# Kernel optimization log

Measured on AMD Instinct MI355X. Metric: run time of the kernel, lower is better.

The kernel has to match this reference:

```python
import jax, jax.numpy as jnp
import numpy as np

K_SIZE = 5
PAD = 2  # (dilation*(k-1)+1 - stride + 1)//2 with k=5, dil=1, stride=1
SAMPLE_NUM = 15
DEPTH_MAX = 192.0


def _gather_patches(x, sample_idx):
    """x: [B,C,H,W] -> [B,H,W,S,C]: values of the 5x5 local neighborhood at the
    SAMPLE_NUM sampled kernel positions (zero padding, matching nn.Unfold)."""
    B, C, H, W = x.shape
    xp = jnp.pad(x, ((0, 0), (0, 0), (PAD, PAD), (PAD, PAD)))
    slabs = []
    for i in range(SAMPLE_NUM):  # small fixed constant, not a data dim
        p = sample_idx[i]
        dy = p // K_SIZE
        dx = p % K_SIZE
        slabs.append(jax.lax.dynamic_slice(xp, (0, 0, dy, dx), (B, C, H, W)))
    pat = jnp.stack(slabs, axis=1)          # [B,S,C,H,W]
    return pat.transpose(0, 3, 4, 1, 2)     # [B,H,W,S,C]


def setup_inputs() -> dict:
    key = jax.random.key(0)
    k1, k2, k3, k4 = jax.random.split(key, 4)
    B, C, H, W = 2, 32, 240, 320
    depth = jax.random.uniform(k1, (B, 1, H, W), dtype=jnp.float32) * 200.0
    surface_normal = jax.random.normal(k2, (B, 3, H, W), dtype=jnp.float32)
    features = jax.random.normal(k3, (B, C, H, W), dtype=jnp.float32)
    guide_weight = jnp.ones((B, H, W, K_SIZE * K_SIZE), dtype=jnp.float32)
    sample_idx = jax.random.randint(k4, (SAMPLE_NUM,), 0, K_SIZE * K_SIZE, dtype=jnp.int32)
    return {"depth": depth, "surface_normal": surface_normal, "features": features,
            "guide_weight": guide_weight, "sample_idx": sample_idx}


def reference(depth, surface_normal, features, guide_weight, sample_idx):
    b, c, h, w = features.shape
    d = depth[:, 0]                                          # squeeze(1) -> [B,H,W]
    valid = ((d > 0) & (d < DEPTH_MAX)).astype(features.dtype)[:, None]  # [B,1,H,W]

    feat_s = _gather_patches(features, sample_idx)           # [B,H,W,S,C]
    norm_s = _gather_patches(surface_normal, sample_idx)     # [B,H,W,S,3]
    valid_s = _gather_patches(valid, sample_idx)[..., 0]     # [B,H,W,S]

    # Faithful to torch: surface_normal.view(b, h, w, 3) is a raw memory
    # reinterpretation, NOT a permute.
    center_n = jnp.reshape(surface_normal, (b, h, w, 3))
    diff = jnp.sqrt(jnp.sum((norm_s - center_n[:, :, :, None, :]) ** 2, axis=-1))
    # torch detaches via the cpu/numpy round-trip -> stop_gradient here
    normal_w = jax.lax.stop_gradient(jnp.exp(-0.5 * diff))   # [B,H,W,S]

    guide_s = jnp.take(guide_weight, sample_idx, axis=3)     # [B,H,W,S]

    fw = valid_s * normal_w * guide_s                        # both weight flags True
    fw = jax.nn.softmax(fw, axis=-1)
    out = jnp.sum(feat_s * fw[..., None], axis=3)            # [B,H,W,C]
    return (out.transpose(0, 3, 1, 2), features)
```

## Files before the change

kernel.cpp:

```cpp
#include <hip/hip_runtime.h>

#define K_SIZE 5
#define PAD 2
#define SAMPLE_NUM 15
#define DEPTH_MAX 192.0f

constexpr int B = 2, C = 32, H = 240, W = 320;
constexpr int HW  = H * W;
constexpr int BHW = B * HW;
constexpr int TOT = B * C * HW;
constexpr int PPB = 128;
constexpr int NBLK = BHW / PPB;
constexpr int XCHUNK = NBLK / 8;

typedef float float4a __attribute__((ext_vector_type(4), aligned(16)));
typedef float float4u __attribute__((ext_vector_type(4), aligned(4)));

__global__ __launch_bounds__(256, 6) void adaptive_sample_fused(
    const float* __restrict__ depth,
    const float* __restrict__ sn,
    const float* __restrict__ features,
    const float* __restrict__ guide,
    const int*   __restrict__ sample_idx,
    float* __restrict__ out,
    float* __restrict__ feat_out)
{
    __shared__ __align__(16) float w_lds[SAMPLE_NUM][PPB];

    const int bid = blockIdx.x;
    const int blk = (bid & 7) * XCHUNK + (bid >> 3);

    const int t    = threadIdx.x;
    const int base = blk * PPB;
    const int b    = base / HW;
    const int pix0 = base - b * HW;

    const float* snb = sn + (size_t)b * 3 * HW;
    const float* db  = depth + (size_t)b * HW;

    {
        const int s  = t & 15;
        const int lq = t >> 4;
        const int pp = sample_idx[(s < SAMPLE_NUM) ? s : 0];
        const int dy = pp / K_SIZE - PAD;
        const int dx = pp - (pp / K_SIZE) * K_SIZE - PAD;

        #pragma unroll
        for (int kk = 0; kk < 8; ++kk) {
            const int lp  = kk * 16 + lq;
            const int pix = pix0 + lp;
            const int y   = pix / W;
            const int x   = pix - y * W;

            const int yy = y + dy, xx = x + dx;
            const bool inb = (s < SAMPLE_NUM) &&
                             (yy >= 0) && (yy < H) && (xx >= 0) && (xx < W);
            const int noff = min(max(yy, 0), H - 1) * W + min(max(xx, 0), W - 1);

            const float d   = db[noff];
            const int   o   = pix * 3;
            const float cn0 = snb[o], cn1 = snb[o + 1], cn2 = snb[o + 2];
            const float d0  = snb[noff]          - cn0;
            const float d1  = snb[HW + noff]     - cn1;
            const float d2  = snb[2 * HW + noff] - cn2;
            const float gv  = guide[((size_t)b * HW + pix) * 25 + pp];

            const float diff = sqrtf(d0 * d0 + d1 * d1 + d2 * d2);
            const bool  ok   = inb && (d > 0.0f) && (d < DEPTH_MAX);
            const float prew = ok ? __expf(-0.5f * diff) * gv : 0.0f;

            float m = prew;
            #pragma unroll
            for (int mask = 1; mask < 16; mask <<= 1)
                m = fmaxf(m, __shfl_xor(m, mask, 16));
            float e = (s < SAMPLE_NUM) ? __expf(prew - m) : 0.0f;
            float sum = e;
            #pragma unroll
            for (int mask = 1; mask < 16; mask <<= 1)
                sum += __shfl_xor(sum, mask, 16);

            if (s < SAMPLE_NUM)
                w_lds[s][lp] = inb ? (e / sum) : 0.0f;
        }
    }
    __syncthreads();

    {
        const int q    = t & 31;
        const int grp  = t >> 5;
        const int ch0  = grp * 4;
        const int pixq = pix0 + 4 * q;
        const int y    = pixq / W;
        const int x    = pixq - y * W;
        const int pb0  = (b * C + ch0) * HW;

        float4a acc[4];
        #pragma unroll
        for (int cc = 0; cc < 4; ++cc) acc[cc] = float4a{0.f, 0.f, 0.f, 0.f};

        #pragma unroll
        for (int s = 0; s < SAMPLE_NUM; ++s) {
            int pp = sample_idx[s];
            int dy = pp / K_SIZE - PAD;
            int dx = pp - (pp / K_SIZE) * K_SIZE - PAD;
            int yy = min(max(y + dy, 0), H - 1);
            int rb = yy * W + x + dx;
            float4a w4 = *(const float4a*)&w_lds[s][4 * q];
            #pragma unroll
            for (int cc = 0; cc < 4; ++cc) {
                int flat = pb0 + cc * HW + rb;
                flat = min(max(flat, 0), TOT - 4);
                float4u f4 = *(const float4u*)(features + flat);
                acc[cc] += w4 * float4a{f4.x, f4.y, f4.z, f4.w};
            }
        }

        const bool fix = (pb0 == 0 && x == 0 && y <= 2) ||
                         (pb0 + 3 * HW == (B * C - 1) * HW && x == W - 4 && y >= H - 3);
        if (fix) {
            #pragma unroll
            for (int cc = 0; cc < 4; ++cc) {
                const float* fpl = features + pb0 + cc * HW;
                float a0 = 0, a1 = 0, a2 = 0, a3 = 0;
                for (int s = 0; s < SAMPLE_NUM; ++s) {
                    int pp = sample_idx[s];
                    int dy = pp / K_SIZE - PAD;
                    int dx = pp - (pp / K_SIZE) * K_SIZE - PAD;
                    int yy = min(max(y + dy, 0), H - 1);
                    const float* frow = fpl + yy * W;
                    int xb = x + dx;
                    a0 += w_lds[s][4 * q + 0] * frow[min(max(xb + 0, 0), W - 1)];
                    a1 += w_lds[s][4 * q + 1] * frow[min(max(xb + 1, 0), W - 1)];
                    a2 += w_lds[s][4 * q + 2] * frow[min(max(xb + 2, 0), W - 1)];
                    a3 += w_lds[s][4 * q + 3] * frow[min(max(xb + 3, 0), W - 1)];
                }
                acc[cc] = float4a{a0, a1, a2, a3};
            }
        }

        #pragma unroll
        for (int cc = 0; cc < 4; ++cc) {
            const int flat = pb0 + cc * HW + pixq;
            float4a pf = *(const float4a*)(features + flat);
            *(float4a*)(out + flat)      = acc[cc];
            *(float4a*)(feat_out + flat) = pf;
        }
    }
}

extern "C" void kernel_launch(void* const* d_in, const int* in_sizes, int n_in,
                              void* d_out, int out_size, void* d_ws, size_t ws_size,
                              hipStream_t stream) {
    const float* depth      = (const float*)d_in[0];
    const float* sn         = (const float*)d_in[1];
    const float* features   = (const float*)d_in[2];
    const float* guide      = (const float*)d_in[3];
    const int*   sample_idx = (const int*)d_in[4];

    float* out      = (float*)d_out;
    float* feat_out = (float*)d_out + (size_t)B * C * HW;

    adaptive_sample_fused<<<NBLK, 256, 0, stream>>>(
        depth, sn, features, guide, sample_idx, out, feat_out);
}
```

Before: 47.98 us.

## Halve pixels per block and batch feature loads per channel

Each block now handles 64 pixels instead of 128, so each thread computes 2 channels rather than 4 and the grid doubles. In the gather phase, all 15 sample loads for a channel are issued into registers before the FMAs, which raises memory-level parallelism, and the row offsets are precomputed once. The occupancy hint drops from 6 to 4 waves to leave room for the larger register footprint. In exchange, the weight-computation work per block shrinks relative to the fixed overhead of each block, and register pressure rises.

New measurement: 43.40 us. 1.11x faster.

```diff
diff --git a/kernel.cpp b/kernel.cpp
--- a/kernel.cpp
+++ b/kernel.cpp
@@ -9,14 +9,14 @@
 constexpr int HW  = H * W;
 constexpr int BHW = B * HW;
 constexpr int TOT = B * C * HW;
-constexpr int PPB = 128;
+constexpr int PPB = 64;
 constexpr int NBLK = BHW / PPB;
 constexpr int XCHUNK = NBLK / 8;
 
 typedef float float4a __attribute__((ext_vector_type(4), aligned(16)));
 typedef float float4u __attribute__((ext_vector_type(4), aligned(4)));
 
-__global__ __launch_bounds__(256, 6) void adaptive_sample_fused(
+__global__ __launch_bounds__(256, 4) void adaptive_sample_fused(
     const float* __restrict__ depth,
     const float* __restrict__ sn,
     const float* __restrict__ features,
@@ -46,7 +46,7 @@
         const int dx = pp - (pp / K_SIZE) * K_SIZE - PAD;
 
         #pragma unroll
-        for (int kk = 0; kk < 8; ++kk) {
+        for (int kk = 0; kk < 4; ++kk) {
             const int lp  = kk * 16 + lq;
             const int pix = pix0 + lp;
             const int y   = pix / W;
@@ -86,40 +86,56 @@
     __syncthreads();
 
     {
-        const int q    = t & 31;
-        const int grp  = t >> 5;
-        const int ch0  = grp * 4;
+        const int q    = t & 15;
+        const int grp  = t >> 4;
+        const int ch0  = grp * 2;
         const int pixq = pix0 + 4 * q;
         const int y    = pixq / W;
         const int x    = pixq - y * W;
         const int pb0  = (b * C + ch0) * HW;
 
-        float4a acc[4];
-        #pragma unroll
-        for (int cc = 0; cc < 4; ++cc) acc[cc] = float4a{0.f, 0.f, 0.f, 0.f};
-
+        int rb[SAMPLE_NUM];
         #pragma unroll
         for (int s = 0; s < SAMPLE_NUM; ++s) {
             int pp = sample_idx[s];
             int dy = pp / K_SIZE - PAD;
             int dx = pp - (pp / K_SIZE) * K_SIZE - PAD;
             int yy = min(max(y + dy, 0), H - 1);
-            int rb = yy * W + x + dx;
-            float4a w4 = *(const float4a*)&w_lds[s][4 * q];
+            rb[s] = yy * W + x + dx;
+        }
+
+        float4a acc0 = {0.f, 0.f, 0.f, 0.f};
+        float4a acc1 = {0.f, 0.f, 0.f, 0.f};
+        {
+            float4a fv[SAMPLE_NUM];
             #pragma unroll
-            for (int cc = 0; cc < 4; ++cc) {
-                int flat = pb0 + cc * HW + rb;
-                flat = min(max(flat, 0), TOT - 4);
+            for (int s = 0; s < SAMPLE_NUM; ++s) {
+                int flat = min(max(pb0 + rb[s], 0), TOT - 4);
                 float4u f4 = *(const float4u*)(features + flat);
-                acc[cc] += w4 * float4a{f4.x, f4.y, f4.z, f4.w};
+                fv[s] = float4a{f4.x, f4.y, f4.z, f4.w};
             }
+            #pragma unroll
+            for (int s = 0; s < SAMPLE_NUM; ++s)
+                acc0 += *(const float4a*)&w_lds[s][4 * q] * fv[s];
+        }
+        {
+            float4a fv[SAMPLE_NUM];
+            #pragma unroll
+            for (int s = 0; s < SAMPLE_NUM; ++s) {
+                int flat = min(max(pb0 + HW + rb[s], 0), TOT - 4);
+                float4u f4 = *(const float4u*)(features + flat);
+                fv[s] = float4a{f4.x, f4.y, f4.z, f4.w};
+            }
+            #pragma unroll
+            for (int s = 0; s < SAMPLE_NUM; ++s)
+                acc1 += *(const float4a*)&w_lds[s][4 * q] * fv[s];
         }
 
         const bool fix = (pb0 == 0 && x == 0 && y <= 2) ||
-                         (pb0 + 3 * HW == (B * C - 1) * HW && x == W - 4 && y >= H - 3);
+                         (pb0 + HW == (B * C - 1) * HW && x == W - 4 && y >= H - 3);
         if (fix) {
             #pragma unroll
-            for (int cc = 0; cc < 4; ++cc) {
+            for (int cc = 0; cc < 2; ++cc) {
                 const float* fpl = features + pb0 + cc * HW;
                 float a0 = 0, a1 = 0, a2 = 0, a3 = 0;
                 for (int s = 0; s < SAMPLE_NUM; ++s) {
@@ -134,17 +150,19 @@
                     a2 += w_lds[s][4 * q + 2] * frow[min(max(xb + 2, 0), W - 1)];
                     a3 += w_lds[s][4 * q + 3] * frow[min(max(xb + 3, 0), W - 1)];
                 }
-                acc[cc] = float4a{a0, a1, a2, a3};
+                if (cc == 0) acc0 = float4a{a0, a1, a2, a3};
+                else         acc1 = float4a{a0, a1, a2, a3};
             }
         }
 
-        #pragma unroll
-        for (int cc = 0; cc < 4; ++cc) {
-            const int flat = pb0 + cc * HW + pixq;
-            float4a pf = *(const float4a*)(features + flat);
-            *(float4a*)(out + flat)      = acc[cc];
-            *(float4a*)(feat_out + flat) = pf;
-        }
+        const int f0 = pb0 + pixq;
+        const int f1 = pb0 + HW + pixq;
+        float4a pf0 = *(const float4a*)(features + f0);
+        float4a pf1 = *(const float4a*)(features + f1);
+        *(float4a*)(out + f0)      = acc0;
+        *(float4a*)(out + f1)      = acc1;
+        *(float4a*)(feat_out + f0) = pf0;
+        *(float4a*)(feat_out + f1) = pf1;
     }
 }
 
```
